# Kernel optimization log

Hardware: AMD Instinct MI355X
Metric: run time of the kernel (lower is better)

Reference implementation:

```python
import jax, jax.numpy as jnp
import numpy as np
import math

B, T, C, H = 4, 1024, 1024, 16
D = C // H
EPS = 1e-5


def layer_norm(x, w, b):
    mu = jnp.mean(x, axis=-1, keepdims=True)
    var = jnp.mean(jnp.square(x - mu), axis=-1, keepdims=True)
    return (x - mu) * jax.lax.rsqrt(var + EPS) * w + b


def setup_inputs() -> dict:
    key = jax.random.key(0)
    ks = jax.random.split(key, 8)
    s = 0.02
    return {
        "x": jax.random.normal(ks[0], (B, T, C), jnp.float32),
        "attention_mask": jnp.ones((B, T), jnp.float32),
        "ln1_w": jnp.ones((C,), jnp.float32),
        "ln1_b": jnp.zeros((C,), jnp.float32),
        "w_attn": jax.random.normal(ks[1], (C, 3 * C), jnp.float32) * s,
        "b_attn": jnp.zeros((3 * C,), jnp.float32),
        "w_proj": jax.random.normal(ks[2], (C, C), jnp.float32) * s,
        "b_proj": jnp.zeros((C,), jnp.float32),
        "threshold": jnp.float32(0.0005),  # (layer_idx+1)/n_layer * final_token_threshold
        "ln2_w": jnp.ones((C,), jnp.float32),
        "ln2_b": jnp.zeros((C,), jnp.float32),
        "w_fc": jax.random.normal(ks[3], (C, 4 * C), jnp.float32) * s,
        "b_fc": jnp.zeros((4 * C,), jnp.float32),
        "w_fc2": jax.random.normal(ks[4], (4 * C, C), jnp.float32) * s,
        "b_fc2": jnp.zeros((C,), jnp.float32),
    }


def reference(x, attention_mask, ln1_w, ln1_b, w_attn, b_attn, w_proj, b_proj,
              threshold, ln2_w, ln2_b, w_fc, b_fc, w_fc2, b_fc2):
    # ---- attention (eval mode, dropout=0; hard masking_mode) ----
    h = layer_norm(x, ln1_w, ln1_b)
    qkv = h @ w_attn + b_attn                      # (B,T,3C)
    q, k, v = jnp.split(qkv, 3, axis=-1)
    q = q.reshape(B, T, H, D).transpose(0, 2, 1, 3)  # (B,H,T,D)
    k = k.reshape(B, T, H, D).transpose(0, 2, 1, 3)
    v = v.reshape(B, T, H, D).transpose(0, 2, 1, 3)

    scale = 1.0 / math.sqrt(D)
    logits = jnp.einsum("bhqd,bhkd->bhqk", q, k) * scale  # (B,H,T,T)
    causal = jnp.tril(jnp.ones((T, T), bool))
    neg_inf = jnp.float32(-jnp.inf)
    logits = jnp.where(causal[None, None], logits, neg_inf)
    # key-side validity mask (applied in original's manual pass; mask is all-ones
    # here so flash-path y == softmax(causal logits) @ v as well)
    logits = jnp.where(attention_mask[:, None, None, :] == 0, neg_inf, logits)
    att = jax.nn.softmax(logits, axis=-1)

    y = jnp.einsum("bhqk,bhkd->bhqd", att, v)      # (B,H,T,D)
    importance = att.mean(axis=1).mean(axis=1)     # (B,T): mean over heads, then queries

    y = y.transpose(0, 2, 1, 3).reshape(B, T, C)
    x = x + (y @ w_proj + b_proj)

    # ---- hard pruning mask ----
    pruning_mask = (importance >= threshold).astype(x.dtype)
    combined_mask = attention_mask * pruning_mask
    x = x * combined_mask[:, :, None]

    # ---- MLP ----
    h2 = layer_norm(x, ln2_w, ln2_b)
    f = jax.nn.gelu(h2 @ w_fc + b_fc, approximate=False)
    x = x + (f @ w_fc2 + b_fc2)

    pruning_loss = jnp.float32(0.0)  # hard mode -> always 0
    return (x, combined_mask, pruning_loss)
```

## Files before the change

### kernel.cpp

```cpp
#include <hip/hip_runtime.h>
#include <cstdint>
#include <cstring>

typedef unsigned short u16;
typedef short bf16x8 __attribute__((ext_vector_type(8)));
typedef float f32x4 __attribute__((ext_vector_type(4)));

#define MFMA16(a,b,c) __builtin_amdgcn_mfma_f32_16x16x32_bf16(a,b,c,0,0,0)


__device__ __forceinline__ u16 f2bf(float f) {
  union { float f; uint32_t u; } un; un.f = f;
  uint32_t u = un.u;
  u += 0x7FFFu + ((u >> 16) & 1u);
  return (u16)(u >> 16);
}

__device__ __forceinline__ float gelu_fast(float v) {
  float u = 0.7978845608028654f * (v + 0.044715f * v * v * v);
  float e = __expf(2.f * u);
  float th = 1.f - __fdividef(2.f, e + 1.f);
  return 0.5f * v * (1.f + th);
}

__device__ __forceinline__ void gl_lds16(const void* g, void* l) {
  __builtin_amdgcn_global_load_lds(
      (__attribute__((address_space(1))) void*)(const_cast<void*>(g)),
      (__attribute__((address_space(3))) void*)l, 16, 0, 0);
}


__global__ __launch_bounds__(256) void transpose_all(
    const float* __restrict__ wa, const float* __restrict__ wp,
    const float* __restrict__ wf, const float* __restrict__ wf2,
    u16* __restrict__ wat, u16* __restrict__ wpt,
    u16* __restrict__ wft, u16* __restrict__ wf2t)
{
  __shared__ float tile[32][33];
  int id = blockIdx.x;
  const float* W; u16* Wt; int K, N, bx, by;
  if (id < 3072)      { W = wa;  Wt = wat;  K = 1024; N = 3072; bx = id % 96;  by = id / 96; }
  else if (id < 4096) { id -= 3072; W = wp;  Wt = wpt;  K = 1024; N = 1024; bx = id % 32; by = id / 32; }
  else if (id < 8192) { id -= 4096; W = wf;  Wt = wft;  K = 1024; N = 4096; bx = id % 128; by = id / 128; }
  else                { id -= 8192; W = wf2; Wt = wf2t; K = 4096; N = 1024; bx = id % 32; by = id / 32; }
  int kt = by * 32, nt = bx * 32;
  int tx = threadIdx.x, ty = threadIdx.y;
#pragma unroll
  for (int i = 0; i < 4; ++i)
    tile[ty + i * 8][tx] = W[(size_t)(kt + ty + i * 8) * N + nt + tx];
  __syncthreads();
#pragma unroll
  for (int i = 0; i < 4; ++i)
    Wt[(size_t)(nt + ty + i * 8) * K + kt + tx] = f2bf(tile[tx][ty + i * 8]);
}


__global__ __launch_bounds__(256) void ln_bf16(
    const float* __restrict__ x, const float* __restrict__ wt,
    const float* __restrict__ bs, u16* __restrict__ out)
{
  int row = blockIdx.x;
  int tid = threadIdx.x, lane = tid & 63, w = tid >> 6;
  const float* xr = x + (size_t)row * 1024;
  float4 v = *(const float4*)(xr + tid * 4);
  float s = v.x + v.y + v.z + v.w;
  float sq = v.x * v.x + v.y * v.y + v.z * v.z + v.w * v.w;
#pragma unroll
  for (int o = 1; o < 64; o <<= 1) { s += __shfl_xor(s, o); sq += __shfl_xor(sq, o); }
  __shared__ float ls[4], lq[4];
  if (lane == 0) { ls[w] = s; lq[w] = sq; }
  __syncthreads();
  s = ls[0] + ls[1] + ls[2] + ls[3];
  sq = lq[0] + lq[1] + lq[2] + lq[3];
  float mu = s * (1.f / 1024.f);
  float var = sq * (1.f / 1024.f) - mu * mu;
  float rstd = rsqrtf(var + 1e-5f);
  float4 wv = *(const float4*)(wt + tid * 4);
  float4 bv = *(const float4*)(bs + tid * 4);
  ushort4 o4;
  o4.x = f2bf((v.x - mu) * rstd * wv.x + bv.x);
  o4.y = f2bf((v.y - mu) * rstd * wv.y + bv.y);
  o4.z = f2bf((v.z - mu) * rstd * wv.z + bv.z);
  o4.w = f2bf((v.w - mu) * rstd * wv.w + bv.w);
  *(ushort4*)(out + (size_t)row * 1024 + tid * 4) = o4;
}


__device__ __forceinline__ void gemm_mainloop_db(
    const u16* __restrict__ Abase, const u16* __restrict__ Bbase,
    int lda, int ldb, int nIter, f32x4 acc[4][4])
{
  __shared__ __align__(16) u16 lA[2][128 * 32];
  __shared__ __align__(16) u16 lB[2][128 * 32];

  const int tid = threadIdx.x;
  const int lane = tid & 63;
  const int w = tid >> 6;
  const int wr = (w >> 1) * 64;
  const int wc = (w & 1) * 64;
  const int laneM = lane & 15;
  const int laneK = (lane >> 4) * 8;

#pragma unroll
  for (int i = 0; i < 4; ++i)
#pragma unroll
    for (int j = 0; j < 4; ++j)
      acc[i][j] = f32x4{0.f, 0.f, 0.f, 0.f};

  const int off0 = w * 1024 + lane * 16;
  const int off1 = off0 + 4096;
  const int rA0 = off0 >> 6, cb0 = off0 & 63;
  const int rA1 = off1 >> 6, cb1 = off1 & 63;

  const size_t sA = (size_t)lda * 2;
  const size_t sB = (size_t)ldb * 2;
  const char* pA0 = (const char*)Abase + (size_t)rA0 * sA + cb0;
  const char* pA1 = (const char*)Abase + (size_t)rA1 * sA + cb1;
  const char* pB0 = (const char*)Bbase + (size_t)rA0 * sB + cb0;
  const char* pB1 = (const char*)Bbase + (size_t)rA1 * sB + cb1;
  char* dA0 = (char*)&lA[0][0] + off0;
  char* dA1 = (char*)&lA[0][0] + off1;
  char* dB0 = (char*)&lB[0][0] + off0;
  char* dB1 = (char*)&lB[0][0] + off1;

  gl_lds16(pA0, dA0); gl_lds16(pA1, dA1);
  gl_lds16(pB0, dB0); gl_lds16(pB1, dB1);
  pA0 += 64; pA1 += 64; pB0 += 64; pB1 += 64;
  __syncthreads();

  for (int it = 0; it < nIter; ++it) {
    const int cur = it & 1;
    const int nb = cur ^ 1;
    if (it + 1 < nIter) {
      gl_lds16(pA0, dA0 + nb * 8192);
      gl_lds16(pA1, dA1 + nb * 8192);
      gl_lds16(pB0, dB0 + nb * 8192);
      gl_lds16(pB1, dB1 + nb * 8192);
      pA0 += 64; pA1 += 64; pB0 += 64; pB1 += 64;
    }
    const u16* aRd = &lA[cur][(wr + laneM) * 32 + laneK];
    const u16* bRd = &lB[cur][(wc + laneM) * 32 + laneK];
    bf16x8 af[4], bfr[4];
#pragma unroll
    for (int t = 0; t < 4; ++t) {
      af[t]  = *(const bf16x8*)(aRd + t * 16 * 32);
      bfr[t] = *(const bf16x8*)(bRd + t * 16 * 32);
    }
#pragma unroll
    for (int i = 0; i < 4; ++i)
#pragma unroll
      for (int j = 0; j < 4; ++j)
        acc[i][j] = MFMA16(af[i], bfr[j], acc[i][j]);
    if (it + 1 < nIter) __syncthreads();
  }
}


__global__ __launch_bounds__(256, 4) void gemm_qkv(
    const u16* __restrict__ A, const u16* __restrict__ Bt,
    const float* __restrict__ bias,
    u16* __restrict__ qo, u16* __restrict__ ko, u16* __restrict__ vo)
{
  f32x4 acc[4][4];
  int m0 = blockIdx.y * 128, n0 = blockIdx.x * 128;
  gemm_mainloop_db(A + (size_t)m0 * 1024, Bt + (size_t)n0 * 1024, 1024, 1024, 32, acc);
  const int lane = threadIdx.x & 63, w = threadIdx.x >> 6;
  const int wr = (w >> 1) * 64, wc = (w & 1) * 64;
  const int laneM = lane & 15, q4 = lane >> 4;
  const int which = (n0 >> 10);
#pragma unroll
  for (int ti = 0; ti < 4; ++ti) {
#pragma unroll
    for (int tj = 0; tj < 4; ++tj) {
      int n = n0 + wc + tj * 16 + laneM;
      int c = n & 1023;
      int hh = c >> 6, d = c & 63;
      float bval = bias[n];
      if (which == 2) {
        int m0r = m0 + wr + ti * 16 + q4 * 4;
        int b = m0r >> 10, t0 = m0r & 1023;
        ushort4 o4;
        o4.x = f2bf(acc[ti][tj][0] + bval);
        o4.y = f2bf(acc[ti][tj][1] + bval);
        o4.z = f2bf(acc[ti][tj][2] + bval);
        o4.w = f2bf(acc[ti][tj][3] + bval);
        *(ushort4*)&vo[((size_t)((b * 16 + hh) * 64 + d)) * 1024 + t0] = o4;
      } else {
        u16* dst = (which == 0) ? qo : ko;
#pragma unroll
        for (int r = 0; r < 4; ++r) {
          int m = m0 + wr + ti * 16 + q4 * 4 + r;
          int b = m >> 10, t = m & 1023;
          dst[((size_t)((b * 16 + hh) * 1024 + t)) * 64 + d] = f2bf(acc[ti][tj][r] + bval);
        }
      }
    }
  }
}

__global__ __launch_bounds__(256, 4) void gemm_proj(
    const u16* __restrict__ A, const u16* __restrict__ Bt,
    const float* __restrict__ bias, const float* __restrict__ xin,
    const float* __restrict__ maskv, float* __restrict__ x2)
{
  f32x4 acc[4][4];
  int m0 = blockIdx.y * 128, n0 = blockIdx.x * 128;
  gemm_mainloop_db(A + (size_t)m0 * 1024, Bt + (size_t)n0 * 1024, 1024, 1024, 32, acc);
  const int lane = threadIdx.x & 63, w = threadIdx.x >> 6;
  const int wr = (w >> 1) * 64, wc = (w & 1) * 64;
  const int laneM = lane & 15, q4 = lane >> 4;
#pragma unroll
  for (int ti = 0; ti < 4; ++ti) {
#pragma unroll
    for (int tj = 0; tj < 4; ++tj) {
      int n = n0 + wc + tj * 16 + laneM;
      float bval = bias[n];
#pragma unroll
      for (int r = 0; r < 4; ++r) {
        int m = m0 + wr + ti * 16 + q4 * 4 + r;
        float v = xin[(size_t)m * 1024 + n] + acc[ti][tj][r] + bval;
        x2[(size_t)m * 1024 + n] = v * maskv[m];
      }
    }
  }
}

__global__ __launch_bounds__(256, 4) void gemm_fc(
    const u16* __restrict__ A, const u16* __restrict__ Bt,
    const float* __restrict__ bias, u16* __restrict__ fo)
{
  f32x4 acc[4][4];
  int m0 = blockIdx.y * 128, n0 = blockIdx.x * 128;
  gemm_mainloop_db(A + (size_t)m0 * 1024, Bt + (size_t)n0 * 1024, 1024, 1024, 32, acc);
  const int lane = threadIdx.x & 63, w = threadIdx.x >> 6;
  const int wr = (w >> 1) * 64, wc = (w & 1) * 64;
  const int laneM = lane & 15, q4 = lane >> 4;
#pragma unroll
  for (int ti = 0; ti < 4; ++ti) {
#pragma unroll
    for (int tj = 0; tj < 4; ++tj) {
      int n = n0 + wc + tj * 16 + laneM;
      float bval = bias[n];
#pragma unroll
      for (int r = 0; r < 4; ++r) {
        int m = m0 + wr + ti * 16 + q4 * 4 + r;
        fo[(size_t)m * 4096 + n] = f2bf(gelu_fast(acc[ti][tj][r] + bval));
      }
    }
  }
}

__global__ __launch_bounds__(256, 4) void gemm_fc2_splitk(
    const u16* __restrict__ A, const u16* __restrict__ Bt,
    float* __restrict__ p0, float* __restrict__ p1)
{
  f32x4 acc[4][4];
  int m0 = blockIdx.y * 128, n0 = blockIdx.x * 128, kz = blockIdx.z;
  gemm_mainloop_db(A + (size_t)m0 * 4096 + kz * 2048,
                   Bt + (size_t)n0 * 4096 + kz * 2048, 4096, 4096, 64, acc);
  float* p = kz ? p1 : p0;
  const int lane = threadIdx.x & 63, w = threadIdx.x >> 6;
  const int wr = (w >> 1) * 64, wc = (w & 1) * 64;
  const int laneM = lane & 15, q4 = lane >> 4;
#pragma unroll
  for (int ti = 0; ti < 4; ++ti) {
#pragma unroll
    for (int tj = 0; tj < 4; ++tj) {
      int n = n0 + wc + tj * 16 + laneM;
#pragma unroll
      for (int r = 0; r < 4; ++r) {
        int m = m0 + wr + ti * 16 + q4 * 4 + r;
        p[(size_t)m * 1024 + n] = acc[ti][tj][r];
      }
    }
  }
}

__global__ __launch_bounds__(256) void fc2_finalize(
    const float* __restrict__ x2, const float* __restrict__ bias,
    const float* __restrict__ p0, const float* __restrict__ p1,
    float* __restrict__ out)
{
  int i = blockIdx.x * 256 + threadIdx.x;
  int col4 = i & 255;
  float4 a = ((const float4*)x2)[i];
  float4 b = ((const float4*)bias)[col4];
  float4 u = ((const float4*)p0)[i];
  float4 v = ((const float4*)p1)[i];
  float4 o;
  o.x = a.x + b.x + u.x + v.x;
  o.y = a.y + b.y + u.y + v.y;
  o.z = a.z + b.z + u.z + v.z;
  o.w = a.w + b.w + u.w + v.w;
  ((float4*)out)[i] = o;
}


__global__ __launch_bounds__(256) void attn_fwd(
    const u16* __restrict__ qb, const u16* __restrict__ kb, const u16* __restrict__ vtb,
    u16* __restrict__ yb, float* __restrict__ part)
{
  const int bh = blockIdx.x;
  const int qbi = 7 - blockIdx.y;
  const int b = bh >> 4, h = bh & 15;
  const int tid = threadIdx.x, lane = tid & 63, w = tid >> 6;
  const int q0 = qbi * 128;
  const int laneM = lane & 15, q4 = lane >> 4;
  const float scale = 0.125f;

  __shared__ __align__(16) u16 lK[64 * 72];
  __shared__ __align__(16) u16 lV[64 * 72];
  __shared__ __align__(16) u16 lP[4][32 * 72];

  bf16x8 qf[2][2];
#pragma unroll
  for (int qs = 0; qs < 2; ++qs) {
    const u16* qrow = qb + ((size_t)(bh * 1024 + q0 + w * 32 + qs * 16 + laneM)) * 64 + q4 * 8;
    qf[qs][0] = *(const bf16x8*)qrow;
    qf[qs][1] = *(const bf16x8*)(qrow + 32);
  }

  const int nkt = 2 * qbi + 2;
  const int srow = tid >> 3;
  const int scol = (tid & 7) * 8;
  const u16* kbase = kb + (size_t)bh * 65536;
  const u16* vbase = vtb + (size_t)bh * 65536;

  float lrow[2][4] = {{0.f,0.f,0.f,0.f},{0.f,0.f,0.f,0.f}};
  for (int kt = 0; kt < nkt; ++kt) {
#pragma unroll
    for (int p = 0; p < 2; ++p) {
      int row = srow + p * 32;
      *(uint4*)&lK[row * 72 + scol] =
          *(const uint4*)(kbase + (size_t)(kt * 64 + row) * 64 + scol);
    }
    __syncthreads();
#pragma unroll
    for (int tj = 0; tj < 4; ++tj) {
      const u16* kp = &lK[(tj * 16 + laneM) * 72 + q4 * 8];
      bf16x8 k0 = *(const bf16x8*)kp;
      bf16x8 k1 = *(const bf16x8*)(kp + 32);
      int kc = kt * 64 + tj * 16 + laneM;
#pragma unroll
      for (int qs = 0; qs < 2; ++qs) {
        f32x4 z = {0.f, 0.f, 0.f, 0.f};
        z = MFMA16(qf[qs][0], k0, z);
        z = MFMA16(qf[qs][1], k1, z);
#pragma unroll
        for (int r = 0; r < 4; ++r) {
          int qg = q0 + w * 32 + qs * 16 + q4 * 4 + r;
          lrow[qs][r] += (kc <= qg) ? __expf(z[r] * scale) : 0.f;
        }
      }
    }
    __syncthreads();
  }
  float linv[2][4];
#pragma unroll
  for (int qs = 0; qs < 2; ++qs)
#pragma unroll
    for (int r = 0; r < 4; ++r) {
      float s = lrow[qs][r];
      s += __shfl_xor(s, 1); s += __shfl_xor(s, 2);
      s += __shfl_xor(s, 4); s += __shfl_xor(s, 8);
      linv[qs][r] = 1.f / s;
    }

  f32x4 o_[2][4];
#pragma unroll
  for (int qs = 0; qs < 2; ++qs)
#pragma unroll
    for (int dt = 0; dt < 4; ++dt) o_[qs][dt] = f32x4{0.f, 0.f, 0.f, 0.f};

  for (int kt = 0; kt < nkt; ++kt) {
#pragma unroll
    for (int p = 0; p < 2; ++p) {
      int row = srow + p * 32;
      *(uint4*)&lK[row * 72 + scol] =
          *(const uint4*)(kbase + (size_t)(kt * 64 + row) * 64 + scol);
      *(uint4*)&lV[row * 72 + scol] =
          *(const uint4*)(vbase + (size_t)row * 1024 + kt * 64 + scol);
    }
    __syncthreads();
    u16* lPw = &lP[w][0];
#pragma unroll
    for (int tj = 0; tj < 4; ++tj) {
      const u16* kp = &lK[(tj * 16 + laneM) * 72 + q4 * 8];
      bf16x8 k0 = *(const bf16x8*)kp;
      bf16x8 k1 = *(const bf16x8*)(kp + 32);
      int kc = kt * 64 + tj * 16 + laneM;
      float cs = 0.f;
#pragma unroll
      for (int qs = 0; qs < 2; ++qs) {
        f32x4 z = {0.f, 0.f, 0.f, 0.f};
        z = MFMA16(qf[qs][0], k0, z);
        z = MFMA16(qf[qs][1], k1, z);
#pragma unroll
        for (int r = 0; r < 4; ++r) {
          int qg = q0 + w * 32 + qs * 16 + q4 * 4 + r;
          float pv = (kc <= qg) ? __expf(z[r] * scale) * linv[qs][r] : 0.f;
          cs += pv;
          lPw[(qs * 16 + q4 * 4 + r) * 72 + tj * 16 + laneM] = f2bf(pv);
        }
      }
      cs += __shfl_xor(cs, 16);
      cs += __shfl_xor(cs, 32);
      if (lane < 16)
        atomicAdd(&part[(size_t)bh * 1024 + kt * 64 + tj * 16 + lane], cs);
    }
#pragma unroll
    for (int ss = 0; ss < 2; ++ss) {
#pragma unroll
      for (int qs = 0; qs < 2; ++qs) {
        bf16x8 pf = *(const bf16x8*)&lP[w][(qs * 16 + laneM) * 72 + ss * 32 + q4 * 8];
#pragma unroll
        for (int dt = 0; dt < 4; ++dt) {
          bf16x8 vf = *(const bf16x8*)&lV[(dt * 16 + laneM) * 72 + ss * 32 + q4 * 8];
          o_[qs][dt] = MFMA16(pf, vf, o_[qs][dt]);
        }
      }
    }
    __syncthreads();
  }

#pragma unroll
  for (int qs = 0; qs < 2; ++qs)
#pragma unroll
    for (int dt = 0; dt < 4; ++dt)
#pragma unroll
      for (int r = 0; r < 4; ++r) {
        int qg = q0 + w * 32 + qs * 16 + q4 * 4 + r;
        yb[((size_t)(b * 1024 + qg)) * 1024 + h * 64 + dt * 16 + laneM] = f2bf(o_[qs][dt][r]);
      }
}


__global__ __launch_bounds__(256) void finalize_mask(
    const float* __restrict__ part, const float* __restrict__ amask,
    const float* __restrict__ thr, float* __restrict__ mask_ws,
    float* __restrict__ out_mask, float* __restrict__ out_loss)
{
  int i = blockIdx.x * 256 + threadIdx.x;
  if (i >= 4096) return;
  int b = i >> 10;
  int t = i & 1023;
  float s = 0.f;
#pragma unroll
  for (int hh = 0; hh < 16; ++hh) s += part[(size_t)(b * 16 + hh) * 1024 + t];
  float imp = s * (1.0f / 16384.0f);
  float mv = (imp >= thr[0]) ? amask[i] : 0.f;
  mask_ws[i] = mv;
  out_mask[i] = mv;
  if (i == 0) out_loss[0] = 0.f;
}


extern "C" void kernel_launch(void* const* d_in, const int* in_sizes, int n_in,
                              void* d_out, int out_size, void* d_ws, size_t ws_size,
                              hipStream_t stream) {
  const float* x      = (const float*)d_in[0];
  const float* amask  = (const float*)d_in[1];
  const float* ln1w   = (const float*)d_in[2];
  const float* ln1b   = (const float*)d_in[3];
  const float* w_attn = (const float*)d_in[4];
  const float* b_attn = (const float*)d_in[5];
  const float* w_proj = (const float*)d_in[6];
  const float* b_proj = (const float*)d_in[7];
  const float* thr    = (const float*)d_in[8];
  const float* ln2w   = (const float*)d_in[9];
  const float* ln2b   = (const float*)d_in[10];
  const float* w_fc   = (const float*)d_in[11];
  const float* b_fc   = (const float*)d_in[12];
  const float* w_fc2  = (const float*)d_in[13];
  const float* b_fc2  = (const float*)d_in[14];
  float* out = (float*)d_out;

  char* ws = (char*)d_ws;
  size_t off = 0;
  auto alloc = [&](size_t bytes) -> char* {
    char* p = ws + off;
    off += (bytes + 255) & ~(size_t)255;
    return p;
  };
  u16* wattnT = (u16*)alloc((size_t)3072 * 1024 * 2);
  u16* wprojT = (u16*)alloc((size_t)1024 * 1024 * 2);
  u16* wfcT   = (u16*)alloc((size_t)4096 * 1024 * 2);
  u16* wfc2T  = (u16*)alloc((size_t)1024 * 4096 * 2);
  u16* hbuf   = (u16*)alloc((size_t)4096 * 1024 * 2);
  u16* qbuf   = (u16*)alloc((size_t)64 * 1024 * 64 * 2);
  u16* kbuf   = (u16*)alloc((size_t)64 * 1024 * 64 * 2);
  u16* vtbuf  = (u16*)alloc((size_t)64 * 64 * 1024 * 2);
  u16* ybuf   = (u16*)alloc((size_t)4096 * 1024 * 2);
  float* part = (float*)alloc((size_t)64 * 1024 * 4);
  float* maskws = (float*)alloc((size_t)4096 * 4);
  float* x2   = (float*)alloc((size_t)4096 * 1024 * 4);
  u16* h2     = (u16*)alloc((size_t)4096 * 1024 * 2);
  u16* fbuf   = (u16*)alloc((size_t)4096 * 4096 * 2);

  float* p0 = (float*)qbuf;
  float* p1 = (float*)vtbuf;

  transpose_all<<<12288, dim3(32, 8), 0, stream>>>(
      w_attn, w_proj, w_fc, w_fc2, wattnT, wprojT, wfcT, wfc2T);

  hipMemsetAsync(part, 0, (size_t)64 * 1024 * 4, stream);

  ln_bf16<<<4096, 256, 0, stream>>>(x, ln1w, ln1b, hbuf);

  gemm_qkv<<<dim3(24, 32), 256, 0, stream>>>(hbuf, wattnT, b_attn, qbuf, kbuf, vtbuf);

  attn_fwd<<<dim3(64, 8), 256, 0, stream>>>(qbuf, kbuf, vtbuf, ybuf, part);

  finalize_mask<<<16, 256, 0, stream>>>(part, amask, thr, maskws,
                                        out + 4194304, out + 4198400);

  gemm_proj<<<dim3(8, 32), 256, 0, stream>>>(ybuf, wprojT, b_proj, x, maskws, x2);

  ln_bf16<<<4096, 256, 0, stream>>>(x2, ln2w, ln2b, h2);

  gemm_fc<<<dim3(32, 32), 256, 0, stream>>>(h2, wfcT, b_fc, fbuf);

  gemm_fc2_splitk<<<dim3(8, 32, 2), 256, 0, stream>>>(fbuf, wfc2T, p0, p1);

  fc2_finalize<<<4096, 256, 0, stream>>>(x2, b_fc2, p0, p1, out);
}
```

Baseline: 375.4 us.

## Split fc2 GEMM four ways with bf16 partials and swizzled block mapping

Raises split-K for the fc2 GEMM from 2 to 4 and launches a 1D grid whose block index is remapped so that neighbouring blocks share M tiles for cache reuse. Partial sums are stored in bf16 instead of fp32, so four partials cost the same write volume as the previous two. The finalize kernel reads and sums all four partials. This gains parallelism and locality at the cost of reduced precision in the partials and an extra partial read in the finalize step.

```diff
diff --git a/kernel.cpp b/kernel.cpp
--- a/kernel.cpp
+++ b/kernel.cpp
@@ -14,6 +14,11 @@
   uint32_t u = un.u;
   u += 0x7FFFu + ((u >> 16) & 1u);
   return (u16)(u >> 16);
+}
+
+__device__ __forceinline__ float bf2f(u16 h) {
+  union { uint32_t u; float f; } un; un.u = ((uint32_t)h) << 16;
+  return un.f;
 }
 
 __device__ __forceinline__ float gelu_fast(float v) {
@@ -252,13 +257,19 @@
 
 __global__ __launch_bounds__(256, 4) void gemm_fc2_splitk(
     const u16* __restrict__ A, const u16* __restrict__ Bt,
-    float* __restrict__ p0, float* __restrict__ p1)
-{
+    u16* __restrict__ pall)
+{
+  int id = blockIdx.x;
+  int r = id & 7, j = id >> 3;
+  int mt = r * 4 + (j >> 5);
+  int rem = j & 31;
+  int n0 = (rem & 7) * 128;
+  int kz = rem >> 3;
+  int m0 = mt * 128;
   f32x4 acc[4][4];
-  int m0 = blockIdx.y * 128, n0 = blockIdx.x * 128, kz = blockIdx.z;
-  gemm_mainloop_db(A + (size_t)m0 * 4096 + kz * 2048,
-                   Bt + (size_t)n0 * 4096 + kz * 2048, 4096, 4096, 64, acc);
-  float* p = kz ? p1 : p0;
+  gemm_mainloop_db(A + (size_t)m0 * 4096 + kz * 1024,
+                   Bt + (size_t)n0 * 4096 + kz * 1024, 4096, 4096, 32, acc);
+  u16* p = pall + (size_t)kz * 4096 * 1024;
   const int lane = threadIdx.x & 63, w = threadIdx.x >> 6;
   const int wr = (w >> 1) * 64, wc = (w & 1) * 64;
   const int laneM = lane & 15, q4 = lane >> 4;
@@ -268,9 +279,9 @@
     for (int tj = 0; tj < 4; ++tj) {
       int n = n0 + wc + tj * 16 + laneM;
 #pragma unroll
-      for (int r = 0; r < 4; ++r) {
-        int m = m0 + wr + ti * 16 + q4 * 4 + r;
-        p[(size_t)m * 1024 + n] = acc[ti][tj][r];
+      for (int r2 = 0; r2 < 4; ++r2) {
+        int m = m0 + wr + ti * 16 + q4 * 4 + r2;
+        p[(size_t)m * 1024 + n] = f2bf(acc[ti][tj][r2]);
       }
     }
   }
@@ -278,20 +289,19 @@
 
 __global__ __launch_bounds__(256) void fc2_finalize(
     const float* __restrict__ x2, const float* __restrict__ bias,
-    const float* __restrict__ p0, const float* __restrict__ p1,
-    float* __restrict__ out)
+    const u16* __restrict__ pall, float* __restrict__ out)
 {
   int i = blockIdx.x * 256 + threadIdx.x;
   int col4 = i & 255;
   float4 a = ((const float4*)x2)[i];
   float4 b = ((const float4*)bias)[col4];
-  float4 u = ((const float4*)p0)[i];
-  float4 v = ((const float4*)p1)[i];
-  float4 o;
-  o.x = a.x + b.x + u.x + v.x;
-  o.y = a.y + b.y + u.y + v.y;
-  o.z = a.z + b.z + u.z + v.z;
-  o.w = a.w + b.w + u.w + v.w;
+  float s0 = a.x + b.x, s1 = a.y + b.y, s2 = a.z + b.z, s3 = a.w + b.w;
+#pragma unroll
+  for (int z = 0; z < 4; ++z) {
+    ushort4 u = ((const ushort4*)(pall + (size_t)z * 4194304))[i];
+    s0 += bf2f(u.x); s1 += bf2f(u.y); s2 += bf2f(u.z); s3 += bf2f(u.w);
+  }
+  float4 o; o.x = s0; o.y = s1; o.z = s2; o.w = s3;
   ((float4*)out)[i] = o;
 }
 
@@ -497,8 +507,7 @@
   u16* h2     = (u16*)alloc((size_t)4096 * 1024 * 2);
   u16* fbuf   = (u16*)alloc((size_t)4096 * 4096 * 2);
 
-  float* p0 = (float*)qbuf;
-  float* p1 = (float*)vtbuf;
+  u16* pall = qbuf;
 
   transpose_all<<<12288, dim3(32, 8), 0, stream>>>(
       w_attn, w_proj, w_fc, w_fc2, wattnT, wprojT, wfcT, wfc2T);
@@ -520,7 +529,7 @@
 
   gemm_fc<<<dim3(32, 32), 256, 0, stream>>>(h2, wfcT, b_fc, fbuf);
 
-  gemm_fc2_splitk<<<dim3(8, 32, 2), 256, 0, stream>>>(fbuf, wfc2T, p0, p1);
-
-  fc2_finalize<<<4096, 256, 0, stream>>>(x2, b_fc2, p0, p1, out);
-}
+  gemm_fc2_splitk<<<1024, 256, 0, stream>>>(fbuf, wfc2T, pall);
+
+  fc2_finalize<<<4096, 256, 0, stream>>>(x2, b_fc2, pall, out);
+}
```

After: 352.8 us. 1.06x faster.
